# Kernel optimization log

Measured on AMD Instinct MI355X. Metric: run time of the kernel, lower is better.

## Reference

```python
import jax, jax.numpy as jnp
import numpy as np

N_FEAT = 512
N_PAIRS = N_FEAT * (N_FEAT - 1) // 2  # 130816


def setup_inputs() -> dict:
    key = jax.random.key(0)
    k1, k2 = jax.random.split(key)
    x = jax.random.normal(k1, (1024, N_FEAT), dtype=jnp.float32)
    weight = jax.random.normal(k2, (N_PAIRS, 1), dtype=jnp.float32) * 0.05  # RandomNormal init
    return {"x": x, "weight": weight}


def reference(x, weight):
    # upper-triangle pair indices (j1 < j2), fixed at trace time
    iu0, iu1 = jnp.triu_indices(N_FEAT, k=1)
    # gather paired features: [B, n_pairs] each; avoid materializing [B, n, n] outer product
    xi = x[:, iu0]
    xj = x[:, iu1]
    # out[b, i] = weight[i] * x[b, j1(i)] * x[b, j2(i)]
    return xi * xj * weight[:, 0][None, :]
```

## Files before the change

kernel.cpp:

```cpp
#include <hip/hip_runtime.h>

#define N_FEAT   512
#define N_PAIRS  130816
#define BROWS    4
#define VEC      4
#define TPB      256
#define PAIRS_PER_BLOCK (TPB * VEC)

__global__ __launch_bounds__(TPB) void widelayer_kernel(
    const float* __restrict__ x,
    const float* __restrict__ w,
    float* __restrict__ out)
{
    __shared__ float xs[BROWS][N_FEAT];
    const int tid   = threadIdx.x;
    const int rbase = blockIdx.y * BROWS;

    const float4* xv  = (const float4*)(x + (long long)rbase * N_FEAT);
    float4*       xsv = (float4*)&xs[0][0];
#pragma unroll
    for (int k = 0; k < (BROWS * N_FEAT / 4) / TPB; ++k)
        xsv[tid + k * TPB] = xv[tid + k * TPB];
    __syncthreads();

    const int p0 = blockIdx.x * PAIRS_PER_BLOCK + tid * VEC;
    if (p0 >= N_PAIRS) return;

    double disc = 1023.0 * 1023.0 - 8.0 * (double)p0;
    int i = (int)((1023.0 - sqrt(disc)) * 0.5);
    if (i < 0) i = 0;
    if (i > 510) i = 510;
    while ((((long long)(i + 1)) * (1023 - (i + 1))) / 2 <= p0 && i < 510) ++i;
    while ((((long long)i) * (1023 - i)) / 2 > p0) --i;
    const long long fi = (((long long)i) * (1023 - i)) / 2;
    int j = i + 1 + (int)(p0 - fi);

    int ii[VEC], jj[VEC];
    int ci = i, cj = j;
#pragma unroll
    for (int k = 0; k < VEC; ++k) {
        ii[k] = ci; jj[k] = cj;
        ++cj;
        if (cj == N_FEAT) { ++ci; cj = ci + 1; }
    }

    const float4 wv = *(const float4*)(w + p0);
    const float wk[VEC] = {wv.x, wv.y, wv.z, wv.w};

#pragma unroll
    for (int r = 0; r < BROWS; ++r) {
        float4 o;
        float* op = (float*)&o;
#pragma unroll
        for (int k = 0; k < VEC; ++k)
            op[k] = (xs[r][ii[k]] * xs[r][jj[k]]) * wk[k];
        *(float4*)(out + (long long)(rbase + r) * N_PAIRS + p0) = o;
    }
}

extern "C" void kernel_launch(void* const* d_in, const int* in_sizes, int n_in,
                              void* d_out, int out_size, void* d_ws, size_t ws_size,
                              hipStream_t stream) {
    const float* x = (const float*)d_in[0];
    const float* w = (const float*)d_in[1];
    float* out = (float*)d_out;

    const int batch = in_sizes[0] / N_FEAT;
    dim3 grid((N_PAIRS + PAIRS_PER_BLOCK - 1) / PAIRS_PER_BLOCK, batch / BROWS);
    widelayer_kernel<<<grid, TPB, 0, stream>>>(x, w, out);
}
```

Before: 513.7 us.

## Use strided scalar pair mapping, float sqrt and nontemporal output stores

Each thread now handles four pairs spaced TPB apart instead of four consecutive pairs. It solves the triangular index per pair in float/int arithmetic instead of double with 64-bit ints, and writes scalar outputs with nontemporal stores. The goal is to drop the slow double-precision sqrt and cut LDS bank conflicts, and to stop the large output stream from polluting the cache. The trade-offs are four index solves per thread instead of one, and scalar loads and stores in place of float4.

```diff
diff --git a/kernel.cpp b/kernel.cpp
--- a/kernel.cpp
+++ b/kernel.cpp
@@ -23,38 +23,38 @@
         xsv[tid + k * TPB] = xv[tid + k * TPB];
     __syncthreads();
 
-    const int p0 = blockIdx.x * PAIRS_PER_BLOCK + tid * VEC;
-    if (p0 >= N_PAIRS) return;
+    const int base = blockIdx.x * PAIRS_PER_BLOCK;
 
-    double disc = 1023.0 * 1023.0 - 8.0 * (double)p0;
-    int i = (int)((1023.0 - sqrt(disc)) * 0.5);
-    if (i < 0) i = 0;
-    if (i > 510) i = 510;
-    while ((((long long)(i + 1)) * (1023 - (i + 1))) / 2 <= p0 && i < 510) ++i;
-    while ((((long long)i) * (1023 - i)) / 2 > p0) --i;
-    const long long fi = (((long long)i) * (1023 - i)) / 2;
-    int j = i + 1 + (int)(p0 - fi);
-
-    int ii[VEC], jj[VEC];
-    int ci = i, cj = j;
+    bool  vk[VEC];
+    int   ii[VEC], jj[VEC];
+    float wk[VEC];
 #pragma unroll
     for (int k = 0; k < VEC; ++k) {
-        ii[k] = ci; jj[k] = cj;
-        ++cj;
-        if (cj == N_FEAT) { ++ci; cj = ci + 1; }
+        vk[k] = (base + k * TPB) < N_PAIRS;
+        int p = vk[k] ? (base + k * TPB + tid) : 0;
+
+        float disc = (float)(1046529 - 8 * p);
+        int i = (int)((1023.0f - sqrtf(disc)) * 0.5f);
+        if (i < 0)   i = 0;
+        if (i > 510) i = 510;
+        while ((i + 1) * (1023 - (i + 1)) / 2 <= p && i < 510) ++i;
+        while (i * (1023 - i) / 2 > p) --i;
+        ii[k] = i;
+        jj[k] = i + 1 + (p - i * (1023 - i) / 2);
+        wk[k] = w[p];
     }
-
-    const float4 wv = *(const float4*)(w + p0);
-    const float wk[VEC] = {wv.x, wv.y, wv.z, wv.w};
 
 #pragma unroll
     for (int r = 0; r < BROWS; ++r) {
-        float4 o;
-        float* op = (float*)&o;
+        const float* xr = xs[r];
+        float* orow = out + (long long)(rbase + r) * N_PAIRS + base + tid;
 #pragma unroll
-        for (int k = 0; k < VEC; ++k)
-            op[k] = (xs[r][ii[k]] * xs[r][jj[k]]) * wk[k];
-        *(float4*)(out + (long long)(rbase + r) * N_PAIRS + p0) = o;
+        for (int k = 0; k < VEC; ++k) {
+            if (vk[k]) {
+                __builtin_nontemporal_store(xr[ii[k]] * xr[jj[k]] * wk[k],
+                                            orow + k * TPB);
+            }
+        }
     }
 }
 
```

Result: slower. 543.2 us (+5.7%).
